# Kernel tuning notes

Measured on AMD Instinct MI355X. Metric: run time of the kernel, lower is better.

The kernel has to match this reference:

```python
import jax, jax.numpy as jnp
import numpy as np
import math

B, S, D, H = 2, 2048, 1024, 16
DK = D // H


def setup_inputs() -> dict:
    key = jax.random.key(0)
    ks = jax.random.split(key, 12)
    scale = 1.0 / math.sqrt(D)
    inp = {
        "q": jax.random.normal(ks[0], (B, S, D), jnp.float32),
        "k": jax.random.normal(ks[1], (B, S, D), jnp.float32),
        "v": jax.random.normal(ks[2], (B, S, D), jnp.float32),
        # causal mask, broadcast over batch and heads; 0 entries are masked out
        "mask": jnp.tril(jnp.ones((S, S), jnp.int32))[None, None, :, :],
        "wq_w": jax.random.normal(ks[3], (D, D), jnp.float32) * scale,
        "wq_b": jax.random.normal(ks[4], (D,), jnp.float32) * 0.01,
        "wk_w": jax.random.normal(ks[5], (D, D), jnp.float32) * scale,
        "wk_b": jax.random.normal(ks[6], (D,), jnp.float32) * 0.01,
        "wv_w": jax.random.normal(ks[7], (D, D), jnp.float32) * scale,
        "wv_b": jax.random.normal(ks[8], (D,), jnp.float32) * 0.01,
        "wo_w": jax.random.normal(ks[9], (D, D), jnp.float32) * scale,
        "wo_b": jax.random.normal(ks[10], (D,), jnp.float32) * 0.01,
    }
    return inp


def _mha(q, k, v, mask, wq_w, wq_b, wk_w, wk_b, wv_w, wv_b, wo_w, wo_b):
    # nn.Linear: x @ W^T + b
    def split_heads(x):  # [B,S,D] -> [B,H,S,DK]
        return x.reshape(B, S, H, DK).transpose(0, 2, 1, 3)

    Q = split_heads(q @ wq_w.T + wq_b)
    K = split_heads(k @ wk_w.T + wk_b)
    V = split_heads(v @ wv_w.T + wv_b)

    scores = jnp.einsum("bhqd,bhkd->bhqk", Q, K) / math.sqrt(DK)  # [B,H,S,S]
    scores = jnp.where(mask == 0, jnp.float32(-1e9), scores)
    # NOTE: source uses softmax(dim=1) == over the HEADS axis; replicated faithfully.
    attn = jax.nn.softmax(scores, axis=1)
    out = jnp.einsum("bhqk,bhkd->bhqd", attn, V)  # [B,H,S,DK]
    out = out.transpose(0, 2, 1, 3).reshape(B, S, D)
    return out @ wo_w.T + wo_b


def reference(q, k, v, mask, wq_w, wq_b, wk_w, wk_b, wv_w, wv_b, wo_w, wo_b):
    return _mha(q, k, v, mask, wq_w, wq_b, wk_w, wk_b, wv_w, wv_b, wo_w, wo_b)
```

## Files before the change

kernel.cpp:

```cpp
#include <hip/hip_runtime.h>
#include <stdint.h>


#define BB 2
#define SS 2048
#define DD 1024
#define HH 16
#define DKK 64

typedef _Float16 f16;
typedef __attribute__((ext_vector_type(2))) _Float16 f16x2;
typedef __attribute__((ext_vector_type(8))) _Float16 f16x8;
typedef __attribute__((ext_vector_type(2))) __fp16 fp16x2_raw;
typedef __attribute__((ext_vector_type(4))) float f32x4;

typedef __attribute__((address_space(3))) uint32_t lds32_t;
typedef __attribute__((address_space(1))) uint32_t g32_t;

__device__ __forceinline__ void async_cp16(void* lds, const void* g){
    __builtin_amdgcn_global_load_lds((const g32_t*)g, (lds32_t*)lds, 16, 0, 0);
}

union U32H { uint32_t u; f16x2 h; fp16x2_raw hr; };

__device__ __forceinline__ uint32_t pk2(float a, float b){
    U32H c; c.hr = __builtin_amdgcn_cvt_pkrtz(a, b); return c.u;
}
__device__ __forceinline__ float h_lo(uint32_t w){ U32H c; c.u = w; return (float)c.h[0]; }
__device__ __forceinline__ float h_hi(uint32_t w){ U32H c; c.u = w; return (float)c.h[1]; }
__device__ __forceinline__ uint32_t pkmul(uint32_t a, uint32_t b){
    U32H x, y, r; x.u = a; y.u = b; r.h = x.h * y.h; return r.u;
}
__device__ __forceinline__ uint16_t f2h(float f){
    union { f16 h; uint16_t u; } c; c.h = (f16)f; return c.u;
}

__global__ __launch_bounds__(256) void cvt_all(
    const float* __restrict__ w0, const float* __restrict__ w1,
    const float* __restrict__ w2, const float* __restrict__ w3,
    const float* __restrict__ a0, const float* __restrict__ a1,
    const float* __restrict__ a2,
    uint16_t* __restrict__ dw0, uint16_t* __restrict__ dw1,
    uint16_t* __restrict__ dw2, uint16_t* __restrict__ dw3,
    uint16_t* __restrict__ da0, uint16_t* __restrict__ da1,
    uint16_t* __restrict__ da2)
{
    const int y = blockIdx.y;
    const float* s; uint16_t* d; int n4;
    switch (y) {
        case 0: s = w0; d = dw0; n4 = 262144; break;
        case 1: s = w1; d = dw1; n4 = 262144; break;
        case 2: s = w2; d = dw2; n4 = 262144; break;
        case 3: s = w3; d = dw3; n4 = 262144; break;
        case 4: s = a0; d = da0; n4 = 1048576; break;
        case 5: s = a1; d = da1; n4 = 1048576; break;
        default: s = a2; d = da2; n4 = 1048576; break;
    }
    int i = blockIdx.x * 256 + threadIdx.x;
    if (i >= n4) return;
    float4 v = ((const float4*)s)[i];
    ((uint2*)d)[i] = make_uint2(pk2(v.x, v.y), pk2(v.z, v.w));
}

template <int OMODE>
__device__ __forceinline__ void gemm_core(
    uint16_t (*As)[32], uint16_t (*Bs)[32],
    const uint16_t* __restrict__ A, const uint16_t* __restrict__ W,
    const float* __restrict__ bias, void* __restrict__ Cout)
{
    const int t    = threadIdx.x;
    const int bm   = blockIdx.x * 128;
    const int bn   = blockIdx.y * 128;
    const int lane = t & 63;
    const int w    = t >> 6;
    const int wm   = (w >> 1) * 64;
    const int wn   = (w & 1) * 64;
    const int lm   = lane & 15;
    const int quad = lane >> 4;

    f32x4 acc[4][4] = {};

    const int lr = lane >> 2;
    const int lc = (lane & 3) * 8;

    for (int k0 = 0; k0 < DD; k0 += 32) {
#pragma unroll
        for (int i2 = 0; i2 < 2; ++i2) {
            const int i = w * 2 + i2;
            async_cp16(&As[16*i][0], &A[(size_t)(bm + 16*i + lr) * DD + k0 + lc]);
            async_cp16(&Bs[16*i][0], &W[(size_t)(bn + 16*i + lr) * DD + k0 + lc]);
        }
        __syncthreads();
        f16x8 a8[4], b8[4];
#pragma unroll
        for (int mt = 0; mt < 4; ++mt) a8[mt] = *(const f16x8*)&As[wm + 16*mt + lm][quad*8];
#pragma unroll
        for (int nt = 0; nt < 4; ++nt) b8[nt] = *(const f16x8*)&Bs[wn + 16*nt + lm][quad*8];
#pragma unroll
        for (int mt = 0; mt < 4; ++mt)
#pragma unroll
            for (int nt = 0; nt < 4; ++nt)
                acc[mt][nt] = __builtin_amdgcn_mfma_f32_16x16x32_f16(a8[mt], b8[nt], acc[mt][nt], 0, 0, 0);
        __syncthreads();
    }

#pragma unroll
    for (int nt = 0; nt < 4; ++nt) {
        const int ng = bn + wn + 16*nt + lm;
        const float bv = bias[ng];
#pragma unroll
        for (int mt = 0; mt < 4; ++mt) {
            const int m0 = bm + wm + 16*mt + quad*4;
            if (OMODE == 1) {
                const int bb = m0 >> 11, s0 = m0 & (SS - 1);
                const int hh = ng >> 6,  dk = ng & 63;
                uint2 wv;
                wv.x = pk2(acc[mt][nt][0] + bv, acc[mt][nt][1] + bv);
                wv.y = pk2(acc[mt][nt][2] + bv, acc[mt][nt][3] + bv);
                *(uint2*)&((uint16_t*)Cout)[(((size_t)(bb*HH + hh))*DKK + dk)*SS + s0] = wv;
            } else {
#pragma unroll
                for (int r = 0; r < 4; ++r) {
                    const int m = m0 + r;
                    const float val = acc[mt][nt][r] + bv;
                    if (OMODE == 0) {
                        const int bb = m >> 11, s = m & (SS - 1);
                        const int hh = ng >> 6, dk = ng & 63;
                        ((uint16_t*)Cout)[(((size_t)(bb*HH + hh))*SS + s)*DKK + dk] = f2h(val);
                    } else {
                        ((float*)Cout)[(size_t)m * DD + ng] = val;
                    }
                }
            }
        }
    }
}

__global__ __launch_bounds__(256) void gemm_qkv(
    const uint16_t* __restrict__ xq, const uint16_t* __restrict__ wq,
    const float* __restrict__ bq, uint16_t* __restrict__ Qc,
    const uint16_t* __restrict__ xk, const uint16_t* __restrict__ wk,
    const float* __restrict__ bk, uint16_t* __restrict__ Kc,
    const uint16_t* __restrict__ xv, const uint16_t* __restrict__ wv,
    const float* __restrict__ bv, uint16_t* __restrict__ Vt)
{
    __shared__ __align__(16) uint16_t As[128][32];
    __shared__ __align__(16) uint16_t Bs[128][32];
    const int z = blockIdx.z;
    if (z == 0)      gemm_core<0>(As, Bs, xq, wq, bq, Qc);
    else if (z == 1) gemm_core<0>(As, Bs, xk, wk, bk, Kc);
    else             gemm_core<1>(As, Bs, xv, wv, bv, Vt);
}

__global__ __launch_bounds__(256) void gemm_o(
    const uint16_t* __restrict__ A, const uint16_t* __restrict__ W,
    const float* __restrict__ bias, float* __restrict__ Cout)
{
    __shared__ __align__(16) uint16_t As[128][32];
    __shared__ __align__(16) uint16_t Bs[128][32];
    gemm_core<2>(As, Bs, A, W, bias, Cout);
}

__global__ __launch_bounds__(256) void suf_kernel(
    const uint16_t* __restrict__ Vt, float* __restrict__ Suf)
{
    const int bh = blockIdx.x;
    const int t  = threadIdx.x;
    const int d = t & 63, seg = t >> 6;
    __shared__ float cs[64][65];
    const uint16_t* row = Vt + ((size_t)bh * DKK + d) * SS;
    for (int cl = 0; cl < 16; ++cl) {
        const int c = seg * 16 + cl;
        float sum = 0.f;
#pragma unroll
        for (int jj = 0; jj < 4; ++jj) {
            uint4 u = *(const uint4*)&row[c * 32 + jj * 8];
            sum += ((h_lo(u.x)+h_hi(u.x)) + (h_lo(u.y)+h_hi(u.y)))
                 + ((h_lo(u.z)+h_hi(u.z)) + (h_lo(u.w)+h_hi(u.w)));
        }
        cs[c][d] = sum;
    }
    __syncthreads();
    if (t < 64) {
        float run = 0.f;
        Suf[((size_t)bh * 65 + 64) * DKK + t] = 0.f;
        for (int c = 63; c >= 0; --c) {
            run += cs[c][t];
            Suf[((size_t)bh * 65 + c) * DKK + t] = run;
        }
    }
}

__global__ __launch_bounds__(1024) void attn_v6(
    const uint16_t* __restrict__ Qc, const uint16_t* __restrict__ Kc,
    const uint16_t* __restrict__ Vt, const float* __restrict__ Suf,
    uint16_t* __restrict__ AOp)
{
    __shared__ __align__(16) uint16_t E[2][16][32][40];
    __shared__ __align__(16) uint16_t Zr[32][40];

    const int x  = blockIdx.x;
    const int p  = x & 3;
    const int b  = (x >> 2) & 1;
    const int pr = x >> 3;
    const int tid  = threadIdx.x;
    const int h    = tid >> 6;
    const int lane = tid & 63;
    const int lm   = lane & 15;
    const int quad = lane >> 4;

    const uint16_t* Qh = Qc + ((size_t)(b*HH + h)) * SS * DKK;
    const uint16_t* Kh = Kc + ((size_t)(b*HH + h)) * SS * DKK;
    const uint16_t* Vh = Vt + ((size_t)(b*HH + h)) * DKK * SS;
    uint16_t* AOb = AOp + ((size_t)(p*BB + b)) * SS * DD;

    const int rq  = tid >> 4;
    const int rk2 = tid & 15;

    int cc = 0;
#pragma unroll
    for (int tt = 0; tt < 2; ++tt) {
        const int tq = tt ? (63 - pr) : pr;
        const int q0 = tq * 32;

        f16x8 qf[2][2];
#pragma unroll
        for (int qt = 0; qt < 2; ++qt)
#pragma unroll
            for (int kd = 0; kd < 2; ++kd)
                qf[qt][kd] = *(const f16x8*)&Qh[(size_t)(q0 + 16*qt + lm)*DKK + kd*32 + quad*8];

        f32x4 oacc[2][4] = {};

        for (int c = p; c <= tq; c += 4, ++cc) {
            const int buf = cc & 1;
            const int k0 = c * 32;
            f16x8 vf[4];
#pragma unroll
            for (int dt = 0; dt < 4; ++dt)
                vf[dt] = *(const f16x8*)&Vh[(size_t)(16*dt + lm)*SS + k0 + quad*8];
            f32x4 sacc[2][2] = {};
#pragma unroll
            for (int kt = 0; kt < 2; ++kt) {
                f16x8 kf0 = *(const f16x8*)&Kh[(size_t)(k0 + 16*kt + lm)*DKK + quad*8];
                f16x8 kf1 = *(const f16x8*)&Kh[(size_t)(k0 + 16*kt + lm)*DKK + 32 + quad*8];
#pragma unroll
                for (int qt = 0; qt < 2; ++qt) {
                    sacc[kt][qt] = __builtin_amdgcn_mfma_f32_16x16x32_f16(kf0, qf[qt][0], sacc[kt][qt], 0, 0, 0);
                    sacc[kt][qt] = __builtin_amdgcn_mfma_f32_16x16x32_f16(kf1, qf[qt][1], sacc[kt][qt], 0, 0, 0);
                }
            }
#pragma unroll
            for (int kt = 0; kt < 2; ++kt)
#pragma unroll
                for (int qt = 0; qt < 2; ++qt) {
                    const int qg = q0 + 16*qt + lm;
                    float e[4];
#pragma unroll
                    for (int r = 0; r < 4; ++r) {
                        const int kg = k0 + 16*kt + quad*4 + r;
                        e[r] = (kg > qg) ? 1.0f : __expf(sacc[kt][qt][r] * 0.125f);
                    }
                    uint2 evw = make_uint2(pk2(e[0], e[1]), pk2(e[2], e[3]));
                    *(uint2*)&E[buf][h][16*qt + lm][16*kt + quad*4] = evw;
                }
            __syncthreads();
            if (tid < 512) {
                float z0 = 0.f, z1 = 0.f;
#pragma unroll
                for (int i = 0; i < 16; ++i) {
                    uint32_t wv2 = *(const uint32_t*)&E[buf][i][rq][rk2*2];
                    z0 += h_lo(wv2); z1 += h_hi(wv2);
                }
                *(uint32_t*)&Zr[rq][rk2*2] = pk2(__fdividef(1.f, z0), __fdividef(1.f, z1));
            }
            __syncthreads();
#pragma unroll
            for (int qt = 0; qt < 2; ++qt) {
                uint4 eu = *(const uint4*)&E[buf][h][16*qt + lm][quad*8];
                uint4 zu = *(const uint4*)&Zr[16*qt + lm][quad*8];
                union { uint4 u; f16x8 v; } P;
                P.u.x = pkmul(eu.x, zu.x); P.u.y = pkmul(eu.y, zu.y);
                P.u.z = pkmul(eu.z, zu.z); P.u.w = pkmul(eu.w, zu.w);
#pragma unroll
                for (int dt = 0; dt < 4; ++dt)
                    oacc[qt][dt] = __builtin_amdgcn_mfma_f32_16x16x32_f16(P.v, vf[dt], oacc[qt][dt], 0, 0, 0);
            }
        }

        float corr[4] = {0.f, 0.f, 0.f, 0.f};
        if (p == 0) {
            const float* Sf = Suf + ((size_t)(b*HH + h) * 65 + (tq + 1)) * DKK;
#pragma unroll
            for (int dt = 0; dt < 4; ++dt) corr[dt] = 0.0625f * Sf[16*dt + lm];
        }
#pragma unroll
        for (int qt = 0; qt < 2; ++qt)
#pragma unroll
            for (int dt = 0; dt < 4; ++dt)
#pragma unroll
                for (int r = 0; r < 4; ++r) {
                    const int s = q0 + 16*qt + quad*4 + r;
                    AOb[(size_t)s * DD + h*DKK + 16*dt + lm] = f2h(oacc[qt][dt][r] + corr[dt]);
                }
    }
}

__global__ __launch_bounds__(256) void reduce4(uint16_t* AOp)
{
    const size_t P1 = (size_t)BB * SS * DD;
    const int i = blockIdx.x * 256 + threadIdx.x;
    uint2 u0 = ((const uint2*)AOp)[i];
    uint2 u1 = ((const uint2*)(AOp + P1))[i];
    uint2 u2 = ((const uint2*)(AOp + 2*P1))[i];
    uint2 u3 = ((const uint2*)(AOp + 3*P1))[i];
    float r0 = (h_lo(u0.x) + h_lo(u1.x)) + (h_lo(u2.x) + h_lo(u3.x));
    float r1 = (h_hi(u0.x) + h_hi(u1.x)) + (h_hi(u2.x) + h_hi(u3.x));
    float r2 = (h_lo(u0.y) + h_lo(u1.y)) + (h_lo(u2.y) + h_lo(u3.y));
    float r3 = (h_hi(u0.y) + h_hi(u1.y)) + (h_hi(u2.y) + h_hi(u3.y));
    ((uint2*)AOp)[i] = make_uint2(pk2(r0, r1), pk2(r2, r3));
}

extern "C" void kernel_launch(void* const* d_in, const int* in_sizes, int n_in,
                              void* d_out, int out_size, void* d_ws, size_t ws_size,
                              hipStream_t stream)
{
    const float* q    = (const float*)d_in[0];
    const float* k    = (const float*)d_in[1];
    const float* v    = (const float*)d_in[2];
    const float* wq_w = (const float*)d_in[4];
    const float* wq_b = (const float*)d_in[5];
    const float* wk_w = (const float*)d_in[6];
    const float* wk_b = (const float*)d_in[7];
    const float* wv_w = (const float*)d_in[8];
    const float* wv_b = (const float*)d_in[9];
    const float* wo_w = (const float*)d_in[10];
    const float* wo_b = (const float*)d_in[11];
    float* out = (float*)d_out;

    uint16_t* wsu = (uint16_t*)d_ws;
    const size_t M1 = (size_t)1 << 20;
    uint16_t* wcq = wsu + 0 * M1;
    uint16_t* wck = wsu + 1 * M1;
    uint16_t* wcv = wsu + 2 * M1;
    uint16_t* wco = wsu + 3 * M1;
    uint16_t* Qc  = wsu + 4 * M1;
    uint16_t* Kc  = wsu + 8 * M1;
    uint16_t* Vt  = wsu + 12 * M1;
    uint16_t* AOp = wsu + 16 * M1;
    uint16_t* xq  = wsu + 16 * M1;
    uint16_t* xk  = wsu + 20 * M1;
    uint16_t* xv  = wsu + 24 * M1;
    float*    Suf = (float*)wcq;

    cvt_all<<<dim3(4096, 7), 256, 0, stream>>>(
        wq_w, wk_w, wv_w, wo_w, q, k, v,
        wcq, wck, wcv, wco, xq, xk, xv);

    gemm_qkv<<<dim3(32, 8, 3), 256, 0, stream>>>(
        xq, wcq, wq_b, Qc,
        xk, wck, wk_b, Kc,
        xv, wcv, wv_b, Vt);

    suf_kernel<<<32, 256, 0, stream>>>(Vt, Suf);
    attn_v6<<<256, 1024, 0, stream>>>(Qc, Kc, Vt, Suf, AOp);

    reduce4<<<4096, 256, 0, stream>>>(AOp);
    gemm_o<<<dim3(32, 8), 256, 0, stream>>>(AOp, wco, wo_b, out);
}
```

Before: 296.5 us.

## Software-pipeline attention chunks with triple-buffered E and split-K output GEMM

The attention kernel now overlaps stages across chunks. In each iteration it computes the cross-head sum for chunk n, the PV product for chunk n-1 and the scores for chunk n+1, using a triple-buffered E array and a double-buffered Zr array. This cuts the barriers per chunk from two to one. The output projection GEMM is split along K into two halves that write fp32 partial buffers, which doubles the block count from 256 to 512 to fill the GPU better, and a new add kernel sums the halves. That adds an extra launch and an extra fp32 read/write pass over the output.

```diff
diff --git a/kernel.cpp b/kernel.cpp
--- a/kernel.cpp
+++ b/kernel.cpp
@@ -66,7 +66,8 @@
 __device__ __forceinline__ void gemm_core(
     uint16_t (*As)[32], uint16_t (*Bs)[32],
     const uint16_t* __restrict__ A, const uint16_t* __restrict__ W,
-    const float* __restrict__ bias, void* __restrict__ Cout)
+    const float* __restrict__ bias, void* __restrict__ Cout,
+    const int kbeg, const int kend)
 {
     const int t    = threadIdx.x;
     const int bm   = blockIdx.x * 128;
@@ -83,7 +84,7 @@
     const int lr = lane >> 2;
     const int lc = (lane & 3) * 8;
 
-    for (int k0 = 0; k0 < DD; k0 += 32) {
+    for (int k0 = kbeg; k0 < kend; k0 += 32) {
 #pragma unroll
         for (int i2 = 0; i2 < 2; ++i2) {
             const int i = w * 2 + i2;
@@ -107,7 +108,7 @@
 #pragma unroll
     for (int nt = 0; nt < 4; ++nt) {
         const int ng = bn + wn + 16*nt + lm;
-        const float bv = bias[ng];
+        const float bv = bias ? bias[ng] : 0.0f;
 #pragma unroll
         for (int mt = 0; mt < 4; ++mt) {
             const int m0 = bm + wm + 16*mt + quad*4;
@@ -147,18 +148,29 @@
     __shared__ __align__(16) uint16_t As[128][32];
     __shared__ __align__(16) uint16_t Bs[128][32];
     const int z = blockIdx.z;
-    if (z == 0)      gemm_core<0>(As, Bs, xq, wq, bq, Qc);
-    else if (z == 1) gemm_core<0>(As, Bs, xk, wk, bk, Kc);
-    else             gemm_core<1>(As, Bs, xv, wv, bv, Vt);
-}
-
-__global__ __launch_bounds__(256) void gemm_o(
+    if (z == 0)      gemm_core<0>(As, Bs, xq, wq, bq, Qc, 0, DD);
+    else if (z == 1) gemm_core<0>(As, Bs, xk, wk, bk, Kc, 0, DD);
+    else             gemm_core<1>(As, Bs, xv, wv, bv, Vt, 0, DD);
+}
+
+__global__ __launch_bounds__(256) void gemm_o_split(
     const uint16_t* __restrict__ A, const uint16_t* __restrict__ W,
-    const float* __restrict__ bias, float* __restrict__ Cout)
+    const float* __restrict__ bias, float* __restrict__ P0, float* __restrict__ P1)
 {
     __shared__ __align__(16) uint16_t As[128][32];
     __shared__ __align__(16) uint16_t Bs[128][32];
-    gemm_core<2>(As, Bs, A, W, bias, Cout);
+    const int z = blockIdx.z;
+    if (z == 0) gemm_core<2>(As, Bs, A, W, bias,    (void*)P0, 0,   512);
+    else        gemm_core<2>(As, Bs, A, W, nullptr, (void*)P1, 512, 1024);
+}
+
+__global__ __launch_bounds__(256) void addf4(
+    const float* __restrict__ a, const float* __restrict__ b, float* __restrict__ o)
+{
+    const int i = blockIdx.x * 256 + threadIdx.x;
+    float4 x = ((const float4*)a)[i];
+    float4 y = ((const float4*)b)[i];
+    ((float4*)o)[i] = make_float4(x.x+y.x, x.y+y.y, x.z+y.z, x.w+y.w);
 }
 
 __global__ __launch_bounds__(256) void suf_kernel(
@@ -191,13 +203,13 @@
     }
 }
 
-__global__ __launch_bounds__(1024) void attn_v6(
+__global__ __launch_bounds__(1024) void attn_v9(
     const uint16_t* __restrict__ Qc, const uint16_t* __restrict__ Kc,
     const uint16_t* __restrict__ Vt, const float* __restrict__ Suf,
     uint16_t* __restrict__ AOp)
 {
-    __shared__ __align__(16) uint16_t E[2][16][32][40];
-    __shared__ __align__(16) uint16_t Zr[32][40];
+    __shared__ __align__(16) uint16_t E[3][16][32][40];
+    __shared__ __align__(16) uint16_t Zr[2][32][40];
 
     const int x  = blockIdx.x;
     const int p  = x & 3;
@@ -217,11 +229,11 @@
     const int rq  = tid >> 4;
     const int rk2 = tid & 15;
 
-    int cc = 0;
 #pragma unroll
     for (int tt = 0; tt < 2; ++tt) {
         const int tq = tt ? (63 - pr) : pr;
         const int q0 = tq * 32;
+        const int nch = (tq >= p) ? ((tq - p) >> 2) + 1 : 0;
 
         f16x8 qf[2][2];
 #pragma unroll
@@ -232,13 +244,8 @@
 
         f32x4 oacc[2][4] = {};
 
-        for (int c = p; c <= tq; c += 4, ++cc) {
-            const int buf = cc & 1;
+        auto SCORES = [&](int c, int ebw) {
             const int k0 = c * 32;
-            f16x8 vf[4];
-#pragma unroll
-            for (int dt = 0; dt < 4; ++dt)
-                vf[dt] = *(const f16x8*)&Vh[(size_t)(16*dt + lm)*SS + k0 + quad*8];
             f32x4 sacc[2][2] = {};
 #pragma unroll
             for (int kt = 0; kt < 2; ++kt) {
@@ -261,24 +268,31 @@
                         const int kg = k0 + 16*kt + quad*4 + r;
                         e[r] = (kg > qg) ? 1.0f : __expf(sacc[kt][qt][r] * 0.125f);
                     }
-                    uint2 evw = make_uint2(pk2(e[0], e[1]), pk2(e[2], e[3]));
-                    *(uint2*)&E[buf][h][16*qt + lm][16*kt + quad*4] = evw;
+                    *(uint2*)&E[ebw][h][16*qt + lm][16*kt + quad*4] =
+                        make_uint2(pk2(e[0], e[1]), pk2(e[2], e[3]));
                 }
-            __syncthreads();
-            if (tid < 512) {
-                float z0 = 0.f, z1 = 0.f;
-#pragma unroll
-                for (int i = 0; i < 16; ++i) {
-                    uint32_t wv2 = *(const uint32_t*)&E[buf][i][rq][rk2*2];
-                    z0 += h_lo(wv2); z1 += h_hi(wv2);
-                }
-                *(uint32_t*)&Zr[rq][rk2*2] = pk2(__fdividef(1.f, z0), __fdividef(1.f, z1));
+        };
+
+        auto HEADSUM = [&](int ebr, int zbw) {
+            float z0 = 0.f, z1 = 0.f;
+#pragma unroll
+            for (int i = 0; i < 16; ++i) {
+                uint32_t wv2 = *(const uint32_t*)&E[ebr][i][rq][rk2*2];
+                z0 += h_lo(wv2); z1 += h_hi(wv2);
             }
-            __syncthreads();
+            *(uint32_t*)&Zr[zbw][rq][rk2*2] = pk2(__fdividef(1.f, z0), __fdividef(1.f, z1));
+        };
+
+        auto PV = [&](int c, int ebr, int zbr) {
+            const int k0 = c * 32;
+            f16x8 vf[4];
+#pragma unroll
+            for (int dt = 0; dt < 4; ++dt)
+                vf[dt] = *(const f16x8*)&Vh[(size_t)(16*dt + lm)*SS + k0 + quad*8];
 #pragma unroll
             for (int qt = 0; qt < 2; ++qt) {
-                uint4 eu = *(const uint4*)&E[buf][h][16*qt + lm][quad*8];
-                uint4 zu = *(const uint4*)&Zr[16*qt + lm][quad*8];
+                uint4 eu = *(const uint4*)&E[ebr][h][16*qt + lm][quad*8];
+                uint4 zu = *(const uint4*)&Zr[zbr][16*qt + lm][quad*8];
                 union { uint4 u; f16x8 v; } P;
                 P.u.x = pkmul(eu.x, zu.x); P.u.y = pkmul(eu.y, zu.y);
                 P.u.z = pkmul(eu.z, zu.z); P.u.w = pkmul(eu.w, zu.w);
@@ -286,6 +300,24 @@
                 for (int dt = 0; dt < 4; ++dt)
                     oacc[qt][dt] = __builtin_amdgcn_mfma_f32_16x16x32_f16(P.v, vf[dt], oacc[qt][dt], 0, 0, 0);
             }
+        };
+
+        __syncthreads();
+
+        if (nch > 0) {
+            SCORES(p, 0);
+            __syncthreads();
+            int eb = 0;
+            for (int n = 0; n < nch; ++n) {
+                const int c  = p + 4*n;
+                const int zb = n & 1;
+                if (tid < 512) HEADSUM(eb, zb);
+                if (n > 0)       PV(c - 4, (eb + 2) % 3, zb ^ 1);
+                if (n + 1 < nch) SCORES(c + 4, (eb + 1) % 3);
+                __syncthreads();
+                eb = (eb + 1 == 3) ? 0 : eb + 1;
+            }
+            PV(p + 4*(nch - 1), (eb + 2) % 3, (nch - 1) & 1);
         }
 
         float corr[4] = {0.f, 0.f, 0.f, 0.f};
@@ -352,6 +384,8 @@
     uint16_t* xk  = wsu + 20 * M1;
     uint16_t* xv  = wsu + 24 * M1;
     float*    Suf = (float*)wcq;
+    float*    P0  = (float*)(wsu + 20 * M1);
+    float*    P1  = (float*)(wsu + 8 * M1);
 
     cvt_all<<<dim3(4096, 7), 256, 0, stream>>>(
         wq_w, wk_w, wv_w, wo_w, q, k, v,
@@ -363,8 +397,9 @@
         xv, wcv, wv_b, Vt);
 
     suf_kernel<<<32, 256, 0, stream>>>(Vt, Suf);
-    attn_v6<<<256, 1024, 0, stream>>>(Qc, Kc, Vt, Suf, AOp);
+    attn_v9<<<256, 1024, 0, stream>>>(Qc, Kc, Vt, Suf, AOp);
 
     reduce4<<<4096, 256, 0, stream>>>(AOp);
-    gemm_o<<<dim3(32, 8), 256, 0, stream>>>(AOp, wco, wo_b, out);
-}
+    gemm_o_split<<<dim3(32, 8, 2), 256, 0, stream>>>(AOp, wco, wo_b, P0, P1);
+    addf4<<<4096, 256, 0, stream>>>(P0, P1, out);
+}
```

Result: faster. 286.2 us (-3.5%).
